# Optimization experiments

Measured on AMD Instinct MI355X. Metric: run time of the kernel, lower is better.

## Reference

```python
import jax, jax.numpy as jnp
import numpy as np

N = 100000
E = 1000000
IN_C, HID, OUT_C = 128, 128, 40
DROPOUT_P = 0.5
BN_EPS = 1e-5


def setup_inputs() -> dict:
    key = jax.random.key(0)
    ks = jax.random.split(key, 10)
    x = jax.random.normal(ks[0], (N, IN_C), dtype=jnp.float32)
    edge_index = jax.random.randint(ks[1], (2, E), 0, N, dtype=jnp.int32)

    def glorot(k, fan_in, fan_out):
        lim = np.sqrt(6.0 / (fan_in + fan_out)).astype(np.float32)
        return jax.random.uniform(k, (fan_in, fan_out), jnp.float32, -lim, lim)

    return {
        "x": x,
        "edge_index": edge_index,
        "W1": glorot(ks[2], IN_C, HID), "b1": jnp.zeros((HID,), jnp.float32),
        "g1": jnp.ones((HID,), jnp.float32), "be1": jnp.zeros((HID,), jnp.float32),
        "W2": glorot(ks[3], HID, HID), "b2": jnp.zeros((HID,), jnp.float32),
        "g2": jnp.ones((HID,), jnp.float32), "be2": jnp.zeros((HID,), jnp.float32),
        "W3": glorot(ks[4], HID, OUT_C), "b3": jnp.zeros((OUT_C,), jnp.float32),
    }


def _deg_inv_sqrt(dst):
    # degree from destination nodes, +1 for the added self loop (PyG gcn_norm)
    deg = jax.ops.segment_sum(jnp.ones((E,), jnp.float32), dst, num_segments=N) + 1.0
    return jax.lax.rsqrt(deg)


def _gcn_conv(h, W, b, src, dst, dinv):
    # h: [N, Cin] -> [N, Cout]; y = D^-1/2 (A + I) D^-1/2 (h W) + b
    hw = h @ W
    norm = dinv[src] * dinv[dst]                      # [E]
    msg = hw[src] * norm[:, None]                     # [E, Cout] gather (memory-bound)
    agg = jax.ops.segment_sum(msg, dst, num_segments=N)
    agg = agg + hw * (dinv * dinv)[:, None]           # self-loop contribution
    return agg + b


def _batchnorm(h, gamma, beta):
    mu = jnp.mean(h, axis=0)
    var = jnp.mean(jnp.square(h - mu), axis=0)        # biased, training mode
    return (h - mu) * jax.lax.rsqrt(var + BN_EPS) * gamma + beta


def _dropout(h, key):
    keep = jax.random.bernoulli(key, 1.0 - DROPOUT_P, h.shape)
    return jnp.where(keep, h / (1.0 - DROPOUT_P), 0.0)


def reference(x, edge_index, W1, b1, g1, be1, W2, b2, g2, be2, W3, b3):
    src, dst = edge_index[0], edge_index[1]
    dinv = _deg_inv_sqrt(dst)
    dk = jax.random.split(jax.random.key(42), 2)

    h = _gcn_conv(x, W1, b1, src, dst, dinv)
    h = _dropout(jax.nn.relu(_batchnorm(h, g1, be1)), dk[0])

    h = _gcn_conv(h, W2, b2, src, dst, dinv)
    h = _dropout(jax.nn.relu(_batchnorm(h, g2, be2)), dk[1])

    h = _gcn_conv(h, W3, b3, src, dst, dinv)
    return jax.nn.log_softmax(h, axis=1)
```

## Files before the change

### kernel.cpp

```cpp
#include <hip/hip_runtime.h>
#include <math.h>

typedef __attribute__((ext_vector_type(8))) short bf16x8;
typedef __attribute__((ext_vector_type(4))) float f32x4;

__device__ __forceinline__ float bfbits2f(unsigned short b){
  return __uint_as_float(((unsigned)b) << 16);
}
__device__ __forceinline__ unsigned short f2bfbits(float f){
  unsigned u = __float_as_uint(f);
  unsigned r = u + 0x7fffu + ((u >> 16) & 1u);
  return (unsigned short)(r >> 16);
}

__host__ __device__ __forceinline__ unsigned rotl32(unsigned v, int d){
  return (v << d) | (v >> (32 - d));
}
__host__ __device__ __forceinline__ void tf2x32(unsigned k0, unsigned k1,
                                                unsigned c0, unsigned c1,
                                                unsigned &o0, unsigned &o1)
{
  unsigned ks2 = k0 ^ k1 ^ 0x1BD11BDAu;
  unsigned x0 = c0 + k0, x1 = c1 + k1;
#define TFR(r) x0 += x1; x1 = rotl32(x1, r); x1 ^= x0;
  TFR(13) TFR(15) TFR(26) TFR(6)
  x0 += k1;  x1 += ks2 + 1u;
  TFR(17) TFR(29) TFR(16) TFR(24)
  x0 += ks2; x1 += k0 + 2u;
  TFR(13) TFR(15) TFR(26) TFR(6)
  x0 += k0;  x1 += k1 + 3u;
  TFR(17) TFR(29) TFR(16) TFR(24)
  x0 += k1;  x1 += ks2 + 4u;
  TFR(13) TFR(15) TFR(26) TFR(6)
  x0 += ks2; x1 += k0 + 5u;
#undef TFR
  o0 = x0; o1 = x1;
}

__global__ __launch_bounds__(256) void k_countpos(const int* __restrict__ dst,
                                                  int* __restrict__ cnt,
                                                  int* __restrict__ pos, int E)
{
  int g = blockIdx.x * 256 + threadIdx.x;
  int base = g * 4;
  if (base + 3 < E){
    int4 d = ((const int4*)dst)[g];
    int4 p;
    p.x = atomicAdd(&cnt[d.x], 1);
    p.y = atomicAdd(&cnt[d.y], 1);
    p.z = atomicAdd(&cnt[d.z], 1);
    p.w = atomicAdd(&cnt[d.w], 1);
    ((int4*)pos)[g] = p;
  } else {
    for (int j = 0; j < 4; j++){
      int e = base + j;
      if (e < E) pos[e] = atomicAdd(&cnt[dst[e]], 1);
    }
  }
}

__global__ __launch_bounds__(256) void k_blocksum(const int* __restrict__ cnt,
                                                  int* __restrict__ bsum, int N)
{
  __shared__ int sh[256];
  int t = threadIdx.x;
  int base = blockIdx.x * 1024 + t * 4;
  int s = 0;
  #pragma unroll
  for (int j = 0; j < 4; j++){ int i = base + j; if (i < N) s += cnt[i]; }
  sh[t] = s; __syncthreads();
  for (int off = 128; off; off >>= 1){
    if (t < off) sh[t] += sh[t + off];
    __syncthreads();
  }
  if (t == 0) bsum[blockIdx.x] = sh[0];
}

__global__ __launch_bounds__(256) void k_scansums(const int* __restrict__ bsum,
                                                  int* __restrict__ boff,
                                                  int* __restrict__ rowstart,
                                                  int NB, int N)
{
  __shared__ int sh[256];
  int t = threadIdx.x;
  int v = (t < NB) ? bsum[t] : 0;
  sh[t] = v; __syncthreads();
  for (int off = 1; off < 256; off <<= 1){
    int x = sh[t];
    int y = (t >= off) ? sh[t - off] : 0;
    __syncthreads();
    sh[t] = x + y;
    __syncthreads();
  }
  if (t < NB) boff[t] = sh[t] - v;
  if (t == NB - 1) rowstart[N] = sh[t];
}

__global__ __launch_bounds__(256) void k_scanfinal(const int* __restrict__ cnt,
                                                   const int* __restrict__ boff,
                                                   int* __restrict__ rowstart,
                                                   float* __restrict__ dinv, int N)
{
  __shared__ int sh[256];
  int t = threadIdx.x;
  int base = blockIdx.x * 1024 + t * 4;
  int c0 = 0, c1 = 0, c2 = 0, c3 = 0;
  if (base + 0 < N) c0 = cnt[base + 0];
  if (base + 1 < N) c1 = cnt[base + 1];
  if (base + 2 < N) c2 = cnt[base + 2];
  if (base + 3 < N) c3 = cnt[base + 3];
  int s = c0 + c1 + c2 + c3;
  sh[t] = s; __syncthreads();
  for (int off = 1; off < 256; off <<= 1){
    int x = sh[t];
    int y = (t >= off) ? sh[t - off] : 0;
    __syncthreads();
    sh[t] = x + y;
    __syncthreads();
  }
  int excl = sh[t] - s + boff[blockIdx.x];
  if (base + 0 < N){ rowstart[base+0] = excl;          dinv[base+0] = rsqrtf((float)c0 + 1.f); }
  if (base + 1 < N){ rowstart[base+1] = excl+c0;       dinv[base+1] = rsqrtf((float)c1 + 1.f); }
  if (base + 2 < N){ rowstart[base+2] = excl+c0+c1;    dinv[base+2] = rsqrtf((float)c2 + 1.f); }
  if (base + 3 < N){ rowstart[base+3] = excl+c0+c1+c2; dinv[base+3] = rsqrtf((float)c3 + 1.f); }
}

__global__ __launch_bounds__(256) void k_fill(const int* __restrict__ src,
                                              const int* __restrict__ dst,
                                              const int* __restrict__ pos,
                                              const int* __restrict__ rowstart,
                                              int* __restrict__ csr, int E)
{
  int g = blockIdx.x * 256 + threadIdx.x;
  int base = g * 4;
  if (base + 3 < E){
    int4 d = ((const int4*)dst)[g];
    int4 p = ((const int4*)pos)[g];
    int4 s = ((const int4*)src)[g];
    int r0 = rowstart[d.x], r1 = rowstart[d.y], r2 = rowstart[d.z], r3 = rowstart[d.w];
    csr[r0 + p.x] = s.x;
    csr[r1 + p.y] = s.y;
    csr[r2 + p.z] = s.z;
    csr[r3 + p.w] = s.w;
  } else {
    for (int j = 0; j < 4; j++){
      int e = base + j;
      if (e < E) csr[rowstart[dst[e]] + pos[e]] = src[e];
    }
  }
}

__global__ __launch_bounds__(256) void k_wt(const float* __restrict__ W1,
                                            const float* __restrict__ W2,
                                            const float* __restrict__ W3,
                                            unsigned short* __restrict__ WT1,
                                            unsigned short* __restrict__ WT2,
                                            unsigned short* __restrict__ WT3)
{
  const float* W; unsigned short* WT; int Cout, Cpad;
  if (blockIdx.x == 0){ W = W1; WT = WT1; Cout = 128; Cpad = 128; }
  else if (blockIdx.x == 1){ W = W2; WT = WT2; Cout = 128; Cpad = 128; }
  else { W = W3; WT = WT3; Cout = 40; Cpad = 48; }
  int tot = Cpad * 136;
  for (int i = threadIdx.x; i < tot; i += 256){
    int n = i / 136, k = i - n * 136;
    float v = (k < 128 && n < Cout) ? W[k * Cout + n] : 0.f;
    WT[i] = f2bfbits(v);
  }
}

template<int NT, int MODE>
__global__ __launch_bounds__(256) void k_gemm_mfma(const void* __restrict__ Ap,
                                                   const unsigned short* __restrict__ WT,
                                                   const float* __restrict__ dinv,
                                                   const float* __restrict__ sums,
                                                   const float* __restrict__ sumsq,
                                                   const float* __restrict__ g,
                                                   const float* __restrict__ be,
                                                   unsigned k0, unsigned k1, float invN,
                                                   unsigned short* __restrict__ outb,
                                                   int N, int Cout)
{
  __shared__ uint4 Wl4[NT * 16 * 17];
  __shared__ uint4 Al4[64 * 16];
  __shared__ float bnS[128], bnB[128];
  unsigned short* Wl = (unsigned short*)Wl4;
  const int t = threadIdx.x;
  const long rb0 = (long)blockIdx.x * 64;

  {
    const uint4* s4 = (const uint4*)WT;
    const int tot = NT * 16 * 17;
    for (int i = t; i < tot; i += 256) Wl4[i] = s4[i];
  }
  if (MODE == 2 && t < 128){
    float mean = sums[t] * invN;
    float var = fmaxf(sumsq[t] * invN - mean * mean, 0.f);
    float rstd = rsqrtf(var + 1e-5f);
    float sc = g[t] * rstd;
    bnS[t] = sc;
    bnB[t] = be[t] - mean * sc;
  }
  if (MODE == 2) __syncthreads();

  #pragma unroll
  for (int i = 0; i < 4; i++){
    int idx = i * 256 + t;
    int r = idx >> 4, c = idx & 15;
    long grow = rb0 + r;
    uint4 chunk = make_uint4(0u, 0u, 0u, 0u);
    if (grow < N){
      if (MODE == 0){
        const float* ap = (const float*)Ap + grow * 128 + c * 8;
        float4 f0 = *(const float4*)ap;
        float4 f1 = *(const float4*)(ap + 4);
        chunk.x = (unsigned)f2bfbits(f0.x) | ((unsigned)f2bfbits(f0.y) << 16);
        chunk.y = (unsigned)f2bfbits(f0.z) | ((unsigned)f2bfbits(f0.w) << 16);
        chunk.z = (unsigned)f2bfbits(f1.x) | ((unsigned)f2bfbits(f1.y) << 16);
        chunk.w = (unsigned)f2bfbits(f1.z) | ((unsigned)f2bfbits(f1.w) << 16);
      } else {
        uint4 raw = *(const uint4*)((const unsigned short*)Ap + grow * 128 + c * 8);
        unsigned idxb = (unsigned)grow * 128u + (unsigned)(c * 8);
        const unsigned* rw = &raw.x;
        unsigned* cw = &chunk.x;
        #pragma unroll
        for (int h = 0; h < 4; h++){
          int ch = c * 8 + 2 * h;
          float f0 = bfbits2f((unsigned short)(rw[h] & 0xffffu));
          float f1 = bfbits2f((unsigned short)(rw[h] >> 16));
          f0 = fmaxf(fmaf(f0, bnS[ch],     bnB[ch]),     0.f);
          f1 = fmaxf(fmaf(f1, bnS[ch + 1], bnB[ch + 1]), 0.f);
          unsigned w0, w1;
          tf2x32(k0, k1, 0u, idxb + 2u * h,      w0, w1);
          f0 = ((w0 ^ w1) & 0x80000000u) ? 0.f : f0 * 2.f;
          tf2x32(k0, k1, 0u, idxb + 2u * h + 1u, w0, w1);
          f1 = ((w0 ^ w1) & 0x80000000u) ? 0.f : f1 * 2.f;
          cw[h] = (unsigned)f2bfbits(f0) | ((unsigned)f2bfbits(f1) << 16);
        }
      }
    }
    Al4[r * 16 + (c ^ (r & 15))] = chunk;
  }
  __syncthreads();

  const int w = t >> 6, l = t & 63;
  const int lm = l & 15, q = l >> 4;

  f32x4 acc[NT];
  #pragma unroll
  for (int nt = 0; nt < NT; nt++){
    acc[nt][0] = 0.f; acc[nt][1] = 0.f; acc[nt][2] = 0.f; acc[nt][3] = 0.f;
  }

  const int arow = w * 16 + lm;
  #pragma unroll
  for (int kt = 0; kt < 4; kt++){
    const int koff = kt * 32 + q * 8;
    bf16x8 a = *(const bf16x8*)&((const unsigned short*)Al4)[arow * 128 + (((kt * 4 + q) ^ lm) * 8)];
    #pragma unroll
    for (int nt = 0; nt < NT; nt++){
      bf16x8 b = *(const bf16x8*)(&Wl[(nt * 16 + lm) * 136 + koff]);
      acc[nt] = __builtin_amdgcn_mfma_f32_16x16x32_bf16(a, b, acc[nt], 0, 0, 0);
    }
  }

  #pragma unroll
  for (int r = 0; r < 4; r++){
    long row = rb0 + w * 16 + q * 4 + r;
    if (row < N){
      float dv = dinv[row];
      #pragma unroll
      for (int nt = 0; nt < NT; nt++){
        int col = nt * 16 + lm;
        if (col < Cout)
          outb[row * Cout + col] = f2bfbits(acc[nt][r] * dv);
      }
    }
  }
}

#define ACC4(U) do{ uint2 _u = (U); \
  a0 += bfbits2f((unsigned short)(_u.x & 0xffffu)); \
  a1 += bfbits2f((unsigned short)(_u.x >> 16)); \
  a2 += bfbits2f((unsigned short)(_u.y & 0xffffu)); \
  a3 += bfbits2f((unsigned short)(_u.y >> 16)); }while(0)

__global__ __launch_bounds__(256) void k_agg128s(const unsigned short* __restrict__ hw,
                                                 const int* __restrict__ rs,
                                                 const int* __restrict__ csr,
                                                 const float* __restrict__ dinv,
                                                 unsigned short* __restrict__ outb,
                                                 float* __restrict__ sums,
                                                 float* __restrict__ sumsq,
                                                 int N)
{
  const int half = (threadIdx.x >> 5) & 1;
  const int sl = threadIdx.x & 31;
  const int ty = threadIdx.y;
  const uint2* h4 = (const uint2*)hw;
  const int base = blockIdx.x * 64;

  float s0 = 0.f, s1 = 0.f, s2 = 0.f, s3 = 0.f;
  float q0 = 0.f, q1 = 0.f, q2 = 0.f, q3 = 0.f;

  #pragma unroll 1
  for (int it = 0; it < 8; it++){
    int v = base + it * 8 + ty * 2 + half;
    if (v < N){
      float a0 = 0.f, a1 = 0.f, a2 = 0.f, a3 = 0.f;
      ACC4(h4[(size_t)v * 32 + sl]);
      int e0 = rs[v], e1 = rs[v + 1];
      int i = e0;
      for (; i + 4 <= e1; i += 4){
        int sa = csr[i], sb = csr[i+1], sc = csr[i+2], sd = csr[i+3];
        uint2 m0 = h4[(size_t)sa * 32 + sl];
        uint2 m1 = h4[(size_t)sb * 32 + sl];
        uint2 m2 = h4[(size_t)sc * 32 + sl];
        uint2 m3 = h4[(size_t)sd * 32 + sl];
        ACC4(m0); ACC4(m1); ACC4(m2); ACC4(m3);
      }
      for (; i < e1; i++){
        ACC4(h4[(size_t)csr[i] * 32 + sl]);
      }
      float dv = dinv[v];
      a0 *= dv; a1 *= dv; a2 *= dv; a3 *= dv;
      uint2 o;
      o.x = (unsigned)f2bfbits(a0) | ((unsigned)f2bfbits(a1) << 16);
      o.y = (unsigned)f2bfbits(a2) | ((unsigned)f2bfbits(a3) << 16);
      ((uint2*)outb)[(size_t)v * 32 + sl] = o;
      s0 += a0; q0 = fmaf(a0, a0, q0);
      s1 += a1; q1 = fmaf(a1, a1, q1);
      s2 += a2; q2 = fmaf(a2, a2, q2);
      s3 += a3; q3 = fmaf(a3, a3, q3);
    }
  }

  __shared__ float shS[8][132], shQ[8][132];
  int grp = ty * 2 + half;
  shS[grp][sl * 4 + 0] = s0; shQ[grp][sl * 4 + 0] = q0;
  shS[grp][sl * 4 + 1] = s1; shQ[grp][sl * 4 + 1] = q1;
  shS[grp][sl * 4 + 2] = s2; shQ[grp][sl * 4 + 2] = q2;
  shS[grp][sl * 4 + 3] = s3; shQ[grp][sl * 4 + 3] = q3;
  __syncthreads();
  int t = ty * 64 + threadIdx.x;
  if (t < 128){
    float ss = 0.f, qq = 0.f;
    #pragma unroll
    for (int g2 = 0; g2 < 8; g2++){ ss += shS[g2][t]; qq += shQ[g2][t]; }
    atomicAdd(&sums[t], ss);
    atomicAdd(&sumsq[t], qq);
  }
}

#define ACC2(U) do{ unsigned _u = (U); \
  acx += bfbits2f((unsigned short)(_u & 0xffffu)); \
  acy += bfbits2f((unsigned short)(_u >> 16)); }while(0)

__global__ __launch_bounds__(256) void k_agg40lsm(const unsigned short* __restrict__ hw,
                                                  const int* __restrict__ rs,
                                                  const int* __restrict__ csr,
                                                  const float* __restrict__ dinv,
                                                  const float* __restrict__ b3,
                                                  float* __restrict__ out, int N)
{
  int half = (threadIdx.x >> 5) & 1;
  int sl = threadIdx.x & 31;
  int v = blockIdx.x * 8 + threadIdx.y * 2 + half;
  bool nact = (v < N);
  bool act = nact && (sl < 20);
  const unsigned* h2 = (const unsigned*)hw;
  float acx = 0.f, acy = 0.f, dv = 1.f;
  if (act){
    dv = dinv[v];
    ACC2(h2[(size_t)v * 20 + sl]);
    int e0 = rs[v], e1 = rs[v + 1];
    int i = e0;
    for (; i + 4 <= e1; i += 4){
      int s0 = csr[i], s1 = csr[i+1], s2 = csr[i+2], s3 = csr[i+3];
      unsigned u0 = h2[(size_t)s0 * 20 + sl];
      unsigned u1 = h2[(size_t)s1 * 20 + sl];
      unsigned u2 = h2[(size_t)s2 * 20 + sl];
      unsigned u3 = h2[(size_t)s3 * 20 + sl];
      ACC2(u0); ACC2(u1); ACC2(u2); ACC2(u3);
    }
    for (; i < e1; i++){
      ACC2(h2[(size_t)csr[i] * 20 + sl]);
    }
  }
  float x0 = act ? fmaf(acx, dv, b3[2 * sl])     : -INFINITY;
  float x1 = act ? fmaf(acy, dv, b3[2 * sl + 1]) : -INFINITY;
  float m = fmaxf(x0, x1);
  #pragma unroll
  for (int off = 16; off; off >>= 1) m = fmaxf(m, __shfl_xor(m, off, 32));
  float e = act ? (expf(x0 - m) + expf(x1 - m)) : 0.f;
  #pragma unroll
  for (int off = 16; off; off >>= 1) e += __shfl_xor(e, off, 32);
  float lse = m + logf(e);
  if (act){
    float2 o; o.x = x0 - lse; o.y = x1 - lse;
    *reinterpret_cast<float2*>(out + (size_t)v * 40 + 2 * sl) = o;
  }
}

extern "C" void kernel_launch(void* const* d_in, const int* in_sizes, int n_in,
                              void* d_out, int out_size, void* d_ws, size_t ws_size,
                              hipStream_t stream)
{
  const float* x  = (const float*)d_in[0];
  const int* ei   = (const int*)d_in[1];
  const float* W1 = (const float*)d_in[2];
  const float* g1 = (const float*)d_in[4];
  const float* be1= (const float*)d_in[5];
  const float* W2 = (const float*)d_in[6];
  const float* g2 = (const float*)d_in[8];
  const float* be2= (const float*)d_in[9];
  const float* W3 = (const float*)d_in[10];
  const float* b3 = (const float*)d_in[11];
  float* out = (float*)d_out;

  const int N = in_sizes[0] / 128;
  const int E = in_sizes[1] / 2;
  const int* srcv = ei;
  const int* dstv = ei + E;

  char* ws = (char*)d_ws;
  size_t off = 0;
  auto take = [&](size_t bytes) -> void* {
    void* p = ws + off;
    off = (off + bytes + 255) & ~(size_t)255;
    return p;
  };
  int*   cnt      = (int*)  take((size_t)N * 4);
  int*   pos      = (int*)  take((size_t)E * 4);
  int*   rowstart = (int*)  take((size_t)(N + 1) * 4);
  int*   csr      = (int*)  take((size_t)E * 4);
  float* dinv     = (float*)take((size_t)N * 4);
  int*   bsum     = (int*)  take(256 * 4);
  int*   boff     = (int*)  take(256 * 4);
  float* sums     = (float*)take(256 * 4);
  float* sumsq    = sums + 128;
  unsigned short* WT1 = (unsigned short*)take(128 * 136 * 2);
  unsigned short* WT2 = (unsigned short*)take(128 * 136 * 2);
  unsigned short* WT3 = (unsigned short*)take(48 * 136 * 2);
  unsigned short* bufX = (unsigned short*)take((size_t)N * 128 * 2);
  unsigned short* bufY = (unsigned short*)take((size_t)N * 128 * 2);
  (void)ws_size; (void)n_in; (void)out_size;

  unsigned l1k0, l1k1, l2k0, l2k1;
  tf2x32(0u, 42u, 0u, 0u, l1k0, l1k1);
  tf2x32(0u, 42u, 0u, 1u, l2k0, l2k1);

  const float invN = 1.0f / (float)N;
  const int NB = (N + 1023) / 1024;
  dim3 wgrid8((N + 7) / 8), wblk(64, 4);
  dim3 wgrid64((N + 63) / 64);
  const int ggrid = (N + 63) / 64;
  const int egrid = (E + 1023) / 1024;

  hipMemsetAsync(cnt, 0, (size_t)N * 4, stream);
  k_countpos<<<egrid, 256, 0, stream>>>(dstv, cnt, pos, E);
  k_blocksum<<<NB, 256, 0, stream>>>(cnt, bsum, N);
  k_scansums<<<1, 256, 0, stream>>>(bsum, boff, rowstart, NB, N);
  k_scanfinal<<<NB, 256, 0, stream>>>(cnt, boff, rowstart, dinv, N);
  k_fill<<<egrid, 256, 0, stream>>>(srcv, dstv, pos, rowstart, csr, E);
  k_wt<<<3, 256, 0, stream>>>(W1, W2, W3, WT1, WT2, WT3);

  k_gemm_mfma<8, 0><<<ggrid, 256, 0, stream>>>(x, WT1, dinv,
      nullptr, nullptr, nullptr, nullptr, 0u, 0u, invN, bufX, N, 128);
  hipMemsetAsync(sums, 0, 256 * 4, stream);
  k_agg128s<<<wgrid64, wblk, 0, stream>>>(bufX, rowstart, csr, dinv, bufY, sums, sumsq, N);

  k_gemm_mfma<8, 2><<<ggrid, 256, 0, stream>>>(bufY, WT2, dinv,
      sums, sumsq, g1, be1, l1k0, l1k1, invN, bufX, N, 128);
  hipMemsetAsync(sums, 0, 256 * 4, stream);
  k_agg128s<<<wgrid64, wblk, 0, stream>>>(bufX, rowstart, csr, dinv, bufY, sums, sumsq, N);

  k_gemm_mfma<3, 2><<<ggrid, 256, 0, stream>>>(bufY, WT3, dinv,
      sums, sumsq, g2, be2, l2k0, l2k1, invN, bufX, N, 40);
  k_agg40lsm<<<wgrid8, wblk, 0, stream>>>(bufX, rowstart, csr, dinv, b3, out, N);
}
```

Baseline: 486.1 us.

## Widen aggregation loads to 16 bytes and spread BN stat atomics over 16 slots

```diff
diff --git a/kernel.cpp b/kernel.cpp
--- a/kernel.cpp
+++ b/kernel.cpp
@@ -173,8 +173,7 @@
 __global__ __launch_bounds__(256) void k_gemm_mfma(const void* __restrict__ Ap,
                                                    const unsigned short* __restrict__ WT,
                                                    const float* __restrict__ dinv,
-                                                   const float* __restrict__ sums,
-                                                   const float* __restrict__ sumsq,
+                                                   const float* __restrict__ stats,
                                                    const float* __restrict__ g,
                                                    const float* __restrict__ be,
                                                    unsigned k0, unsigned k1, float invN,
@@ -194,8 +193,14 @@
     for (int i = t; i < tot; i += 256) Wl4[i] = s4[i];
   }
   if (MODE == 2 && t < 128){
-    float mean = sums[t] * invN;
-    float var = fmaxf(sumsq[t] * invN - mean * mean, 0.f);
+    float ss = 0.f, qq = 0.f;
+    #pragma unroll
+    for (int i = 0; i < 16; i++){
+      ss += stats[i * 256 + t];
+      qq += stats[i * 256 + 128 + t];
+    }
+    float mean = ss * invN;
+    float var = fmaxf(qq * invN - mean * mean, 0.f);
     float rstd = rsqrtf(var + 1e-5f);
     float sc = g[t] * rstd;
     bnS[t] = sc;
@@ -279,76 +284,83 @@
   }
 }
 
-#define ACC4(U) do{ uint2 _u = (U); \
+#define ACC8(U) do{ uint4 _u = (U); \
   a0 += bfbits2f((unsigned short)(_u.x & 0xffffu)); \
   a1 += bfbits2f((unsigned short)(_u.x >> 16)); \
   a2 += bfbits2f((unsigned short)(_u.y & 0xffffu)); \
-  a3 += bfbits2f((unsigned short)(_u.y >> 16)); }while(0)
+  a3 += bfbits2f((unsigned short)(_u.y >> 16)); \
+  a4 += bfbits2f((unsigned short)(_u.z & 0xffffu)); \
+  a5 += bfbits2f((unsigned short)(_u.z >> 16)); \
+  a6 += bfbits2f((unsigned short)(_u.w & 0xffffu)); \
+  a7 += bfbits2f((unsigned short)(_u.w >> 16)); }while(0)
 
 __global__ __launch_bounds__(256) void k_agg128s(const unsigned short* __restrict__ hw,
                                                  const int* __restrict__ rs,
                                                  const int* __restrict__ csr,
                                                  const float* __restrict__ dinv,
                                                  unsigned short* __restrict__ outb,
-                                                 float* __restrict__ sums,
-                                                 float* __restrict__ sumsq,
+                                                 float* __restrict__ stats,
                                                  int N)
 {
-  const int half = (threadIdx.x >> 5) & 1;
-  const int sl = threadIdx.x & 31;
+  const int l = threadIdx.x;
+  const int ns = l >> 4;
+  const int sl = l & 15;
   const int ty = threadIdx.y;
-  const uint2* h4 = (const uint2*)hw;
-  const int base = blockIdx.x * 64;
-
-  float s0 = 0.f, s1 = 0.f, s2 = 0.f, s3 = 0.f;
-  float q0 = 0.f, q1 = 0.f, q2 = 0.f, q3 = 0.f;
+  const int grp = ty * 4 + ns;
+  const uint4* h16 = (const uint4*)hw;
+  const int base = blockIdx.x * 32;
+
+  float s0=0.f,s1=0.f,s2=0.f,s3=0.f,s4=0.f,s5=0.f,s6=0.f,s7=0.f;
+  float q0=0.f,q1=0.f,q2=0.f,q3=0.f,q4=0.f,q5=0.f,q6=0.f,q7=0.f;
 
   #pragma unroll 1
-  for (int it = 0; it < 8; it++){
-    int v = base + it * 8 + ty * 2 + half;
+  for (int it = 0; it < 2; it++){
+    int v = base + it * 16 + grp;
     if (v < N){
-      float a0 = 0.f, a1 = 0.f, a2 = 0.f, a3 = 0.f;
-      ACC4(h4[(size_t)v * 32 + sl]);
+      float a0=0.f,a1=0.f,a2=0.f,a3=0.f,a4=0.f,a5=0.f,a6=0.f,a7=0.f;
+      ACC8(h16[(size_t)v * 16 + sl]);
       int e0 = rs[v], e1 = rs[v + 1];
       int i = e0;
       for (; i + 4 <= e1; i += 4){
         int sa = csr[i], sb = csr[i+1], sc = csr[i+2], sd = csr[i+3];
-        uint2 m0 = h4[(size_t)sa * 32 + sl];
-        uint2 m1 = h4[(size_t)sb * 32 + sl];
-        uint2 m2 = h4[(size_t)sc * 32 + sl];
-        uint2 m3 = h4[(size_t)sd * 32 + sl];
-        ACC4(m0); ACC4(m1); ACC4(m2); ACC4(m3);
+        uint4 m0 = h16[(size_t)sa * 16 + sl];
+        uint4 m1 = h16[(size_t)sb * 16 + sl];
+        uint4 m2 = h16[(size_t)sc * 16 + sl];
+        uint4 m3 = h16[(size_t)sd * 16 + sl];
+        ACC8(m0); ACC8(m1); ACC8(m2); ACC8(m3);
       }
       for (; i < e1; i++){
-        ACC4(h4[(size_t)csr[i] * 32 + sl]);
+        ACC8(h16[(size_t)csr[i] * 16 + sl]);
       }
       float dv = dinv[v];
-      a0 *= dv; a1 *= dv; a2 *= dv; a3 *= dv;
-      uint2 o;
+      a0*=dv; a1*=dv; a2*=dv; a3*=dv; a4*=dv; a5*=dv; a6*=dv; a7*=dv;
+      uint4 o;
       o.x = (unsigned)f2bfbits(a0) | ((unsigned)f2bfbits(a1) << 16);
       o.y = (unsigned)f2bfbits(a2) | ((unsigned)f2bfbits(a3) << 16);
-      ((uint2*)outb)[(size_t)v * 32 + sl] = o;
-      s0 += a0; q0 = fmaf(a0, a0, q0);
-      s1 += a1; q1 = fmaf(a1, a1, q1);
-      s2 += a2; q2 = fmaf(a2, a2, q2);
-      s3 += a3; q3 = fmaf(a3, a3, q3);
-    }
-  }
-
-  __shared__ float shS[8][132], shQ[8][132];
-  int grp = ty * 2 + half;
-  shS[grp][sl * 4 + 0] = s0; shQ[grp][sl * 4 + 0] = q0;
-  shS[grp][sl * 4 + 1] = s1; shQ[grp][sl * 4 + 1] = q1;
-  shS[grp][sl * 4 + 2] = s2; shQ[grp][sl * 4 + 2] = q2;
-  shS[grp][sl * 4 + 3] = s3; shQ[grp][sl * 4 + 3] = q3;
+      o.z = (unsigned)f2bfbits(a4) | ((unsigned)f2bfbits(a5) << 16);
+      o.w = (unsigned)f2bfbits(a6) | ((unsigned)f2bfbits(a7) << 16);
+      ((uint4*)outb)[(size_t)v * 16 + sl] = o;
+      s0+=a0; q0=fmaf(a0,a0,q0);  s1+=a1; q1=fmaf(a1,a1,q1);
+      s2+=a2; q2=fmaf(a2,a2,q2);  s3+=a3; q3=fmaf(a3,a3,q3);
+      s4+=a4; q4=fmaf(a4,a4,q4);  s5+=a5; q5=fmaf(a5,a5,q5);
+      s6+=a6; q6=fmaf(a6,a6,q6);  s7+=a7; q7=fmaf(a7,a7,q7);
+    }
+  }
+
+  __shared__ float shS[16][128], shQ[16][128];
+  *(float4*)&shS[grp][sl * 8]     = make_float4(s0, s1, s2, s3);
+  *(float4*)&shS[grp][sl * 8 + 4] = make_float4(s4, s5, s6, s7);
+  *(float4*)&shQ[grp][sl * 8]     = make_float4(q0, q1, q2, q3);
+  *(float4*)&shQ[grp][sl * 8 + 4] = make_float4(q4, q5, q6, q7);
   __syncthreads();
   int t = ty * 64 + threadIdx.x;
   if (t < 128){
     float ss = 0.f, qq = 0.f;
     #pragma unroll
-    for (int g2 = 0; g2 < 8; g2++){ ss += shS[g2][t]; qq += shQ[g2][t]; }
-    atomicAdd(&sums[t], ss);
-    atomicAdd(&sumsq[t], qq);
+    for (int g2 = 0; g2 < 16; g2++){ ss += shS[g2][t]; qq += shQ[g2][t]; }
+    float* dstat = stats + (blockIdx.x & 15) * 256;
+    atomicAdd(&dstat[t], ss);
+    atomicAdd(&dstat[128 + t], qq);
   }
 }
 
@@ -437,8 +449,7 @@
   float* dinv     = (float*)take((size_t)N * 4);
   int*   bsum     = (int*)  take(256 * 4);
   int*   boff     = (int*)  take(256 * 4);
-  float* sums     = (float*)take(256 * 4);
-  float* sumsq    = sums + 128;
+  float* stats    = (float*)take(16 * 256 * 4);
   unsigned short* WT1 = (unsigned short*)take(128 * 136 * 2);
   unsigned short* WT2 = (unsigned short*)take(128 * 136 * 2);
   unsigned short* WT3 = (unsigned short*)take(48 * 136 * 2);
@@ -453,7 +464,7 @@
   const float invN = 1.0f / (float)N;
   const int NB = (N + 1023) / 1024;
   dim3 wgrid8((N + 7) / 8), wblk(64, 4);
-  dim3 wgrid64((N + 63) / 64);
+  dim3 wgrid32((N + 31) / 32);
   const int ggrid = (N + 63) / 64;
   const int egrid = (E + 1023) / 1024;
 
@@ -466,16 +477,16 @@
   k_wt<<<3, 256, 0, stream>>>(W1, W2, W3, WT1, WT2, WT3);
 
   k_gemm_mfma<8, 0><<<ggrid, 256, 0, stream>>>(x, WT1, dinv,
-      nullptr, nullptr, nullptr, nullptr, 0u, 0u, invN, bufX, N, 128);
-  hipMemsetAsync(sums, 0, 256 * 4, stream);
-  k_agg128s<<<wgrid64, wblk, 0, stream>>>(bufX, rowstart, csr, dinv, bufY, sums, sumsq, N);
+      nullptr, nullptr, nullptr, 0u, 0u, invN, bufX, N, 128);
+  hipMemsetAsync(stats, 0, 16 * 256 * 4, stream);
+  k_agg128s<<<wgrid32, wblk, 0, stream>>>(bufX, rowstart, csr, dinv, bufY, stats, N);
 
   k_gemm_mfma<8, 2><<<ggrid, 256, 0, stream>>>(bufY, WT2, dinv,
-      sums, sumsq, g1, be1, l1k0, l1k1, invN, bufX, N, 128);
-  hipMemsetAsync(sums, 0, 256 * 4, stream);
-  k_agg128s<<<wgrid64, wblk, 0, stream>>>(bufX, rowstart, csr, dinv, bufY, sums, sumsq, N);
+      stats, g1, be1, l1k0, l1k1, invN, bufX, N, 128);
+  hipMemsetAsync(stats, 0, 16 * 256 * 4, stream);
+  k_agg128s<<<wgrid32, wblk, 0, stream>>>(bufX, rowstart, csr, dinv, bufY, stats, N);
 
   k_gemm_mfma<3, 2><<<ggrid, 256, 0, stream>>>(bufY, WT3, dinv,
-      sums, sumsq, g2, be2, l2k0, l2k1, invN, bufX, N, 40);
+      stats, g2, be2, l2k0, l2k1, invN, bufX, N, 40);
   k_agg40lsm<<<wgrid8, wblk, 0, stream>>>(bufX, rowstart, csr, dinv, b3, out, N);
 }
```

Result: faster. 422.5 us (-13.1%).
